# Kernel optimization log

Hardware: AMD Instinct MI355X
Metric: run time of the kernel (lower is better)

Reference implementation:

```python
import jax, jax.numpy as jnp
import numpy as np

NUM_HEADS = 16
HEAD_DIM = 64  # hidden_size 1024 / 16 heads


def setup_inputs() -> dict:
    key = jax.random.key(0)
    ks = jax.random.split(key, 4)
    B, S, H = 2, 2048, 1024
    scale = 0.02
    return {
        "hidden_states": jax.random.normal(ks[0], (B, S, H), jnp.float32),
        "attention_mask": jnp.zeros((B, 1, 1, S), jnp.float32),  # additive mask
        "Wq": jax.random.normal(ks[1], (H, H), jnp.float32) * scale,
        "bq": jnp.zeros((H,), jnp.float32),
        "Wk": jax.random.normal(ks[2], (H, H), jnp.float32) * scale,
        "bk": jnp.zeros((H,), jnp.float32),
        "Wv": jax.random.normal(ks[3], (H, H), jnp.float32) * scale,
        "bv": jnp.zeros((H,), jnp.float32),
    }


def _split_heads(x):
    B, S, H = x.shape
    return x.reshape(B, S, NUM_HEADS, HEAD_DIM).transpose(0, 2, 1, 3)  # [B,h,S,dh]


def reference(hidden_states, attention_mask, Wq, bq, Wk, bk, Wv, bv):
    q = _split_heads(hidden_states @ Wq + bq)
    k = _split_heads(hidden_states @ Wk + bk)
    v = _split_heads(hidden_states @ Wv + bv)
    # scaled dot-product scores [B,h,S,S]
    scores = jnp.einsum("bhqd,bhkd->bhqk", q, k) / np.sqrt(HEAD_DIM).astype(np.float32)
    scores = scores + attention_mask  # additive mask, broadcast [B,1,1,S]
    probs = jax.nn.softmax(scores, axis=-1)  # dropout prob = 0.0
    ctx = jnp.einsum("bhqk,bhkd->bhqd", probs, v)
    B, h, S, dh = ctx.shape
    return ctx.transpose(0, 2, 1, 3).reshape(B, S, h * dh)  # [B,S,hidden]
```

## Files before the change

### kernel.cpp

```cpp
#include <hip/hip_runtime.h>
#include <hip/hip_bf16.h>


typedef __bf16 bf16x8 __attribute__((ext_vector_type(8)));
typedef __bf16 bf16x4 __attribute__((ext_vector_type(4)));
typedef float f32x4 __attribute__((ext_vector_type(4)));
typedef float f32x16 __attribute__((ext_vector_type(16)));

static constexpr int H = 1024;
static constexpr int S = 2048;
static constexpr int NH = 16;
static constexpr int DH = 64;
static constexpr float L2E = 1.4426950408889634f;

#if __has_builtin(__builtin_amdgcn_exp2f)
#define EXP2F(x) __builtin_amdgcn_exp2f(x)
#else
#define EXP2F(x) __builtin_exp2f(x)
#endif

__device__ inline void gll16(const void* g, void* l) {
  __builtin_amdgcn_global_load_lds(
      (const __attribute__((address_space(1))) void*)g,
      (__attribute__((address_space(3))) void*)l, 16, 0, 0);
}

__global__ __launch_bounds__(256) void convert_kernel(
    const float* __restrict__ X, const float* __restrict__ W0,
    const float* __restrict__ W1, const float* __restrict__ W2,
    __bf16* __restrict__ Xb, __bf16* __restrict__ Wt) {
  __shared__ float T[64][65];
  const int bid = blockIdx.x, tid = threadIdx.x;
  if (bid < 2048) {
    size_t i = ((size_t)bid * 256 + tid) * 8;
    float4 f0 = *(const float4*)(X + i);
    float4 f1 = *(const float4*)(X + i + 4);
    bf16x8 o;
    o[0] = (__bf16)f0.x; o[1] = (__bf16)f0.y; o[2] = (__bf16)f0.z; o[3] = (__bf16)f0.w;
    o[4] = (__bf16)f1.x; o[5] = (__bf16)f1.y; o[6] = (__bf16)f1.z; o[7] = (__bf16)f1.w;
    *(bf16x8*)(Xb + i) = o;
    return;
  }
  const int wid = bid - 2048;
  const int z = wid >> 8, t = wid & 255;
  const int k0 = (t >> 4) * 64, n0 = (t & 15) * 64;
  const float* W = z == 0 ? W0 : (z == 1 ? W1 : W2);
  __bf16* Wo = Wt + (size_t)z * H * H;
#pragma unroll
  for (int it = 0; it < 4; ++it) {
    int r = it * 16 + (tid >> 4), c = (tid & 15) * 4;
    *(float4*)&T[r][c] = *(const float4*)&W[(size_t)(k0 + r) * H + n0 + c];
  }
  __syncthreads();
#pragma unroll
  for (int it = 0; it < 4; ++it) {
    int n = it * 16 + (tid >> 4), c0 = (tid & 15) * 4;
    bf16x4 o;
#pragma unroll
    for (int j = 0; j < 4; ++j) o[j] = (__bf16)T[c0 + j][n];
    *(bf16x4*)&Wo[(size_t)(n0 + n) * H + k0 + c0] = o;
  }
}

__global__ __launch_bounds__(256, 3) void qkv_gemm_kernel(
    const __bf16* __restrict__ Xb, const __bf16* __restrict__ Wt,
    const float* __restrict__ bq, const float* __restrict__ bk,
    const float* __restrict__ bv,
    __bf16* __restrict__ Qt, __bf16* __restrict__ K, __bf16* __restrict__ Vt)
{
  __shared__ __bf16 As[128 * 64];
  __shared__ __bf16 Bs[128 * 64];

  const int tid = threadIdx.x, lane = tid & 63, w = tid >> 6;
  const int quad = lane >> 4, l16 = lane & 15;
  const int wsel = blockIdx.x >> 3;
  const int n0 = (blockIdx.x & 7) * 128;
  const int m0 = blockIdx.y * 128;
  const int wr = w & 1, wc = w >> 1;

  const __bf16* Wsel = Wt + (size_t)wsel * H * H;
  const float* bias = wsel == 0 ? bq : (wsel == 1 ? bk : bv);

  const __bf16* aptr[4];
  const __bf16* bptr[4];
#pragma unroll
  for (int i = 0; i < 4; ++i) {
    int s = w * 256 + i * 64 + lane;
    int row = s >> 3, col = s & 7, sc = col ^ (row & 7);
    aptr[i] = Xb + (size_t)(m0 + row) * H + sc * 8;
    bptr[i] = Wsel + (size_t)(n0 + row) * H + sc * 8;
  }

  f32x4 acc[4][4] = {};

  for (int k0 = 0; k0 < H; k0 += 64) {
    __syncthreads();
#pragma unroll
    for (int i = 0; i < 4; ++i) {
      gll16(aptr[i] + k0, &As[(w * 256 + i * 64) * 8]);
      gll16(bptr[i] + k0, &Bs[(w * 256 + i * 64) * 8]);
    }
    __syncthreads();
#pragma unroll
    for (int kc = 0; kc < 2; ++kc) {
      bf16x8 af[4], bfr[4];
#pragma unroll
      for (int t = 0; t < 4; ++t) {
        int ra = wr * 64 + t * 16 + l16;
        af[t] = *(const bf16x8*)&As[ra * 64 + (((kc * 4 + quad) ^ (ra & 7)) * 8)];
        int rb = wc * 64 + t * 16 + l16;
        bfr[t] = *(const bf16x8*)&Bs[rb * 64 + (((kc * 4 + quad) ^ (rb & 7)) * 8)];
      }
#pragma unroll
      for (int t = 0; t < 4; ++t)
#pragma unroll
        for (int u = 0; u < 4; ++u)
          acc[t][u] = __builtin_amdgcn_mfma_f32_16x16x32_bf16(af[t], bfr[u], acc[t][u], 0, 0, 0);
    }
  }

  const float qscale = 0.125f * L2E;
#pragma unroll
  for (int u = 0; u < 4; ++u) {
    int n = n0 + wc * 64 + u * 16 + l16;
    int head = n >> 6, d = n & 63;
    float bias_v = bias[n];
#pragma unroll
    for (int t = 0; t < 4; ++t) {
      int srow = m0 + wr * 64 + t * 16 + quad * 4;
      int b = srow >> 11, si = srow & (S - 1);
      int bh = b * NH + head;
      if (wsel == 1) {
        __bf16* dst = K + ((size_t)bh * S + si) * DH + d;
#pragma unroll
        for (int r = 0; r < 4; ++r)
          dst[(size_t)r * DH] = (__bf16)(acc[t][u][r] + bias_v);
      } else {
        float scl = wsel == 0 ? qscale : 1.0f;
        __bf16* outp = wsel == 0 ? Qt : Vt;
        bf16x4 o;
#pragma unroll
        for (int r = 0; r < 4; ++r) o[r] = (__bf16)((acc[t][u][r] + bias_v) * scl);
        *(bf16x4*)&outp[((size_t)bh * DH + d) * S + si] = o;
      }
    }
  }
}

__global__ __launch_bounds__(256, 2) void attn_kernel(
    const __bf16* __restrict__ Qt, const __bf16* __restrict__ K,
    const __bf16* __restrict__ Vt, const float* __restrict__ mask,
    float* __restrict__ out)
{
  __shared__ __bf16 Ks[2][64 * 64];
  __shared__ __bf16 Vs[2][64 * 64];
  __shared__ float  Ms[S];
  __shared__ __bf16 Pb[4][32 * 64];

  const int tid = threadIdx.x, lane = tid & 63, w = tid >> 6;
  const int l31 = lane & 31, hi = lane >> 5;

  const int lin = blockIdx.y * 16 + blockIdx.x;
  const int v = (lin & 7) * 64 + (lin >> 3);
  const int bh = v >> 4, b = bh >> 4, h = bh & 15;
  const int q0 = (v & 15) * 128;

  const __bf16* Qb = Qt + (size_t)bh * DH * S;
  const __bf16* Kb = K + (size_t)bh * S * DH;
  const __bf16* Vb = Vt + (size_t)bh * DH * S;
  const float* mb = mask + (size_t)b * S;

  {
    int idx = tid * 8;
    float4 m0v = *(const float4*)&mb[idx];
    float4 m1v = *(const float4*)&mb[idx + 4];
    float4 s0v = {m0v.x * L2E, m0v.y * L2E, m0v.z * L2E, m0v.w * L2E};
    float4 s1v = {m1v.x * L2E, m1v.y * L2E, m1v.z * L2E, m1v.w * L2E};
    *(float4*)&Ms[idx] = s0v;
    *(float4*)&Ms[idx + 4] = s1v;
  }

  const int q = q0 + w * 32 + l31;
  bf16x8 qf[4];
#pragma unroll
  for (int kc = 0; kc < 4; ++kc)
#pragma unroll
    for (int j = 0; j < 8; ++j)
      qf[kc][j] = Qb[(size_t)(kc * 16 + hi * 8 + j) * S + q];

  const __bf16* kptr[2];
  const __bf16* vptr[2];
#pragma unroll
  for (int i = 0; i < 2; ++i) {
    int s = w * 128 + i * 64 + lane;
    int row = s >> 3, col = s & 7, sc = col ^ (row & 7);
    kptr[i] = Kb + (size_t)row * DH + sc * 8;
    vptr[i] = Vb + (size_t)row * S + sc * 8;
  }

#pragma unroll
  for (int i = 0; i < 2; ++i) {
    gll16(kptr[i], &Ks[0][(w * 128 + i * 64) * 8]);
    gll16(vptr[i], &Vs[0][(w * 128 + i * 64) * 8]);
  }

  f32x16 o0 = {}, o1 = {};
  float dl = 0.0f;
  int cur = 0;

  for (int kv0 = 0; kv0 < S; kv0 += 64) {
    __syncthreads();
    if (kv0 + 64 < S) {
      const int nxt = cur ^ 1;
#pragma unroll
      for (int i = 0; i < 2; ++i) {
        gll16(kptr[i] + (size_t)(kv0 + 64) * DH, &Ks[nxt][(w * 128 + i * 64) * 8]);
        gll16(vptr[i] + (kv0 + 64), &Vs[nxt][(w * 128 + i * 64) * 8]);
      }
    }

#pragma unroll
    for (int kvsub = 0; kvsub < 2; ++kvsub) {
      const int rk = kvsub * 32 + l31;
      f32x16 cc;
#pragma unroll
      for (int g = 0; g < 4; ++g) {
        float4 m4 = *(const float4*)&Ms[kv0 + kvsub * 32 + g * 8 + hi * 4];
        cc[4 * g + 0] = m4.x; cc[4 * g + 1] = m4.y;
        cc[4 * g + 2] = m4.z; cc[4 * g + 3] = m4.w;
      }
#pragma unroll
      for (int kc = 0; kc < 4; ++kc) {
        bf16x8 af = *(const bf16x8*)&Ks[cur][rk * 64 + (((kc * 2 + hi) ^ (l31 & 7)) * 8)];
        cc = __builtin_amdgcn_mfma_f32_32x32x16_bf16(af, qf[kc], cc, 0, 0, 0);
      }
#pragma unroll
      for (int g = 0; g < 4; ++g) {
        bf16x4 pk;
#pragma unroll
        for (int r = 0; r < 4; ++r) {
          float p = EXP2F(cc[4 * g + r]);
          pk[r] = (__bf16)p;
          dl += (float)pk[r];
        }
        int ccn = kvsub * 4 + g;
        *(bf16x4*)&Pb[w][l31 * 64 + ((ccn ^ (l31 & 7)) * 8) + hi * 4] = pk;
      }
    }

    bf16x8 pf[4];
#pragma unroll
    for (int pc = 0; pc < 4; ++pc)
      pf[pc] = *(const bf16x8*)&Pb[w][l31 * 64 + (((pc * 2 + hi) ^ (l31 & 7)) * 8)];
#pragma unroll
    for (int pc = 0; pc < 4; ++pc) {
      bf16x8 vf0 = *(const bf16x8*)&Vs[cur][l31 * 64 + (((pc * 2 + hi) ^ (l31 & 7)) * 8)];
      o0 = __builtin_amdgcn_mfma_f32_32x32x16_bf16(vf0, pf[pc], o0, 0, 0, 0);
      bf16x8 vf1 = *(const bf16x8*)&Vs[cur][(32 + l31) * 64 + (((pc * 2 + hi) ^ (l31 & 7)) * 8)];
      o1 = __builtin_amdgcn_mfma_f32_32x32x16_bf16(vf1, pf[pc], o1, 0, 0, 0);
    }
    cur ^= 1;
  }

  float lsum = dl + __shfl_xor(dl, 32);
  float invl = 1.0f / lsum;

#pragma unroll
  for (int g = 0; g < 4; ++g) {
    int d0 = g * 8 + hi * 4;
    float4 s0 = {o0[4 * g + 0] * invl, o0[4 * g + 1] * invl,
                 o0[4 * g + 2] * invl, o0[4 * g + 3] * invl};
    *(float4*)&out[((size_t)b * S + q) * H + h * DH + d0] = s0;
    float4 s1 = {o1[4 * g + 0] * invl, o1[4 * g + 1] * invl,
                 o1[4 * g + 2] * invl, o1[4 * g + 3] * invl};
    *(float4*)&out[((size_t)b * S + q) * H + h * DH + 32 + d0] = s1;
  }
}

extern "C" void kernel_launch(void* const* d_in, const int* in_sizes, int n_in,
                              void* d_out, int out_size, void* d_ws, size_t ws_size,
                              hipStream_t stream) {
  const float* X    = (const float*)d_in[0];
  const float* mask = (const float*)d_in[1];
  const float* Wq   = (const float*)d_in[2];
  const float* bq   = (const float*)d_in[3];
  const float* Wk   = (const float*)d_in[4];
  const float* bk   = (const float*)d_in[5];
  const float* Wv   = (const float*)d_in[6];
  const float* bv   = (const float*)d_in[7];
  float* out = (float*)d_out;

  const size_t per = (size_t)2 * NH * S * DH;
  __bf16* Qws  = (__bf16*)d_ws;
  __bf16* Kws  = Qws + per;
  __bf16* Vtws = Kws + per;

  __bf16* Xb = (__bf16*)d_out;
  __bf16* Wt = Xb + per;

  convert_kernel<<<2816, 256, 0, stream>>>(X, Wq, Wk, Wv, Xb, Wt);
  qkv_gemm_kernel<<<dim3(24, 32), 256, 0, stream>>>(Xb, Wt, bq, bk, bv,
                                                    Qws, Kws, Vtws);
  attn_kernel<<<dim3(16, 32), 256, 0, stream>>>(Qws, Kws, Vtws, mask, out);
}
```

Measured before the change: 173.8 us.

## Split KV range across two wave groups and pass P through registers via permlane swap

The attention block grows to 512 threads. Two groups of four waves each process half of the KV sequence and their partial outputs and row sums are merged through LDS at the end. The P matrix is no longer staged through LDS; it is packed into bf16 pairs and rearranged across lanes with v_permlane32_swap so it can feed the PV MFMA directly. s_setprio hints are added around the MFMA sections. The aim is more waves in flight per query tile and less LDS traffic, at the cost of an extra reduction step, more LDS per block, and tighter register limits from launch_bounds(512,4).

```diff
diff --git a/kernel.cpp b/kernel.cpp
--- a/kernel.cpp
+++ b/kernel.cpp
@@ -6,6 +6,7 @@
 typedef __bf16 bf16x4 __attribute__((ext_vector_type(4)));
 typedef float f32x4 __attribute__((ext_vector_type(4)));
 typedef float f32x16 __attribute__((ext_vector_type(16)));
+typedef int i32x4 __attribute__((ext_vector_type(4)));
 
 static constexpr int H = 1024;
 static constexpr int S = 2048;
@@ -23,6 +24,16 @@
   __builtin_amdgcn_global_load_lds(
       (const __attribute__((address_space(1))) void*)g,
       (__attribute__((address_space(3))) void*)l, 16, 0, 0);
+}
+
+__device__ inline int pack2bf(float lo, float hi) {
+  unsigned short a = __builtin_bit_cast(unsigned short, (__bf16)lo);
+  unsigned short b = __builtin_bit_cast(unsigned short, (__bf16)hi);
+  return (int)(((unsigned)b << 16) | (unsigned)a);
+}
+
+__device__ inline void plswap(int& a, int& b) {
+  asm volatile("v_permlane32_swap_b32 %0, %1" : "+v"(a), "+v"(b));
 }
 
 __global__ __launch_bounds__(256) void convert_kernel(
@@ -147,18 +158,18 @@
   }
 }
 
-__global__ __launch_bounds__(256, 2) void attn_kernel(
+__global__ __launch_bounds__(512, 4) void attn_kernel(
     const __bf16* __restrict__ Qt, const __bf16* __restrict__ K,
     const __bf16* __restrict__ Vt, const float* __restrict__ mask,
     float* __restrict__ out)
 {
-  __shared__ __bf16 Ks[2][64 * 64];
-  __shared__ __bf16 Vs[2][64 * 64];
+  __shared__ __bf16 Ks[2][2][64 * 64];
+  __shared__ __bf16 Vs[2][2][64 * 64];
   __shared__ float  Ms[S];
-  __shared__ __bf16 Pb[4][32 * 64];
 
   const int tid = threadIdx.x, lane = tid & 63, w = tid >> 6;
   const int l31 = lane & 31, hi = lane >> 5;
+  const int wl = w & 3, wh = w >> 2;
 
   const int lin = blockIdx.y * 16 + blockIdx.x;
   const int v = (lin & 7) * 64 + (lin >> 3);
@@ -171,16 +182,13 @@
   const float* mb = mask + (size_t)b * S;
 
   {
-    int idx = tid * 8;
-    float4 m0v = *(const float4*)&mb[idx];
-    float4 m1v = *(const float4*)&mb[idx + 4];
-    float4 s0v = {m0v.x * L2E, m0v.y * L2E, m0v.z * L2E, m0v.w * L2E};
-    float4 s1v = {m1v.x * L2E, m1v.y * L2E, m1v.z * L2E, m1v.w * L2E};
-    *(float4*)&Ms[idx] = s0v;
-    *(float4*)&Ms[idx + 4] = s1v;
-  }
-
-  const int q = q0 + w * 32 + l31;
+    int idx = tid * 4;
+    float4 mv = *(const float4*)&mb[idx];
+    float4 sv = {mv.x * L2E, mv.y * L2E, mv.z * L2E, mv.w * L2E};
+    *(float4*)&Ms[idx] = sv;
+  }
+
+  const int q = q0 + wl * 32 + l31;
   bf16x8 qf[4];
 #pragma unroll
   for (int kc = 0; kc < 4; ++kc)
@@ -188,36 +196,40 @@
     for (int j = 0; j < 8; ++j)
       qf[kc][j] = Qb[(size_t)(kc * 16 + hi * 8 + j) * S + q];
 
+  const int kvbase = wh * 1024;
   const __bf16* kptr[2];
   const __bf16* vptr[2];
 #pragma unroll
   for (int i = 0; i < 2; ++i) {
-    int s = w * 128 + i * 64 + lane;
+    int s = wl * 128 + i * 64 + lane;
     int row = s >> 3, col = s & 7, sc = col ^ (row & 7);
-    kptr[i] = Kb + (size_t)row * DH + sc * 8;
-    vptr[i] = Vb + (size_t)row * S + sc * 8;
+    kptr[i] = Kb + (size_t)(kvbase + row) * DH + sc * 8;
+    vptr[i] = Vb + (size_t)row * S + kvbase + sc * 8;
   }
 
 #pragma unroll
   for (int i = 0; i < 2; ++i) {
-    gll16(kptr[i], &Ks[0][(w * 128 + i * 64) * 8]);
-    gll16(vptr[i], &Vs[0][(w * 128 + i * 64) * 8]);
+    gll16(kptr[i], &Ks[wh][0][(wl * 128 + i * 64 + lane) * 8]);
+    gll16(vptr[i], &Vs[wh][0][(wl * 128 + i * 64 + lane) * 8]);
   }
 
   f32x16 o0 = {}, o1 = {};
   float dl = 0.0f;
   int cur = 0;
 
-  for (int kv0 = 0; kv0 < S; kv0 += 64) {
+  for (int st = 0; st < 16; ++st) {
     __syncthreads();
-    if (kv0 + 64 < S) {
+    if (st + 1 < 16) {
       const int nxt = cur ^ 1;
 #pragma unroll
       for (int i = 0; i < 2; ++i) {
-        gll16(kptr[i] + (size_t)(kv0 + 64) * DH, &Ks[nxt][(w * 128 + i * 64) * 8]);
-        gll16(vptr[i] + (kv0 + 64), &Vs[nxt][(w * 128 + i * 64) * 8]);
-      }
-    }
+        gll16(kptr[i] + (size_t)(st + 1) * 64 * DH, &Ks[wh][nxt][(wl * 128 + i * 64 + lane) * 8]);
+        gll16(vptr[i] + (st + 1) * 64, &Vs[wh][nxt][(wl * 128 + i * 64 + lane) * 8]);
+      }
+    }
+    const __bf16* Kc = &Ks[wh][cur][0];
+    const __bf16* Vc = &Vs[wh][cur][0];
+    const int kvabs = kvbase + st * 64;
 
 #pragma unroll
     for (int kvsub = 0; kvsub < 2; ++kvsub) {
@@ -225,55 +237,82 @@
       f32x16 cc;
 #pragma unroll
       for (int g = 0; g < 4; ++g) {
-        float4 m4 = *(const float4*)&Ms[kv0 + kvsub * 32 + g * 8 + hi * 4];
+        float4 m4 = *(const float4*)&Ms[kvabs + kvsub * 32 + g * 8 + hi * 4];
         cc[4 * g + 0] = m4.x; cc[4 * g + 1] = m4.y;
         cc[4 * g + 2] = m4.z; cc[4 * g + 3] = m4.w;
       }
+      __builtin_amdgcn_s_setprio(1);
 #pragma unroll
       for (int kc = 0; kc < 4; ++kc) {
-        bf16x8 af = *(const bf16x8*)&Ks[cur][rk * 64 + (((kc * 2 + hi) ^ (l31 & 7)) * 8)];
+        bf16x8 af = *(const bf16x8*)&Kc[rk * 64 + (((kc * 2 + hi) ^ (l31 & 7)) * 8)];
         cc = __builtin_amdgcn_mfma_f32_32x32x16_bf16(af, qf[kc], cc, 0, 0, 0);
       }
-#pragma unroll
-      for (int g = 0; g < 4; ++g) {
-        bf16x4 pk;
-#pragma unroll
-        for (int r = 0; r < 4; ++r) {
-          float p = EXP2F(cc[4 * g + r]);
-          pk[r] = (__bf16)p;
-          dl += (float)pk[r];
-        }
-        int ccn = kvsub * 4 + g;
-        *(bf16x4*)&Pb[w][l31 * 64 + ((ccn ^ (l31 & 7)) * 8) + hi * 4] = pk;
-      }
-    }
-
-    bf16x8 pf[4];
-#pragma unroll
-    for (int pc = 0; pc < 4; ++pc)
-      pf[pc] = *(const bf16x8*)&Pb[w][l31 * 64 + (((pc * 2 + hi) ^ (l31 & 7)) * 8)];
-#pragma unroll
-    for (int pc = 0; pc < 4; ++pc) {
-      bf16x8 vf0 = *(const bf16x8*)&Vs[cur][l31 * 64 + (((pc * 2 + hi) ^ (l31 & 7)) * 8)];
-      o0 = __builtin_amdgcn_mfma_f32_32x32x16_bf16(vf0, pf[pc], o0, 0, 0, 0);
-      bf16x8 vf1 = *(const bf16x8*)&Vs[cur][(32 + l31) * 64 + (((pc * 2 + hi) ^ (l31 & 7)) * 8)];
-      o1 = __builtin_amdgcn_mfma_f32_32x32x16_bf16(vf1, pf[pc], o1, 0, 0, 0);
+      __builtin_amdgcn_s_setprio(0);
+
+      float p[16];
+#pragma unroll
+      for (int r = 0; r < 16; ++r) { p[r] = EXP2F(cc[r]); dl += p[r]; }
+      int a0 = pack2bf(p[0],  p[1]),  b0 = pack2bf(p[2],  p[3]);
+      int a1 = pack2bf(p[4],  p[5]),  b1 = pack2bf(p[6],  p[7]);
+      int a2 = pack2bf(p[8],  p[9]),  b2 = pack2bf(p[10], p[11]);
+      int a3 = pack2bf(p[12], p[13]), b3 = pack2bf(p[14], p[15]);
+      plswap(a0, a1); plswap(b0, b1);
+      plswap(a2, a3); plswap(b2, b3);
+      i32x4 pi0 = {a0, b0, a1, b1};
+      i32x4 pi1 = {a2, b2, a3, b3};
+      bf16x8 pf0 = __builtin_bit_cast(bf16x8, pi0);
+      bf16x8 pf1 = __builtin_bit_cast(bf16x8, pi1);
+
+      __builtin_amdgcn_s_setprio(1);
+#pragma unroll
+      for (int pp = 0; pp < 2; ++pp) {
+        const int pc = kvsub * 2 + pp;
+        const bf16x8 pf = pp ? pf1 : pf0;
+        bf16x8 vf0 = *(const bf16x8*)&Vc[l31 * 64 + (((pc * 2 + hi) ^ (l31 & 7)) * 8)];
+        o0 = __builtin_amdgcn_mfma_f32_32x32x16_bf16(vf0, pf, o0, 0, 0, 0);
+        bf16x8 vf1 = *(const bf16x8*)&Vc[(32 + l31) * 64 + (((pc * 2 + hi) ^ (l31 & 7)) * 8)];
+        o1 = __builtin_amdgcn_mfma_f32_32x32x16_bf16(vf1, pf, o1, 0, 0, 0);
+      }
+      __builtin_amdgcn_s_setprio(0);
     }
     cur ^= 1;
   }
 
   float lsum = dl + __shfl_xor(dl, 32);
-  float invl = 1.0f / lsum;
-
-#pragma unroll
-  for (int g = 0; g < 4; ++g) {
-    int d0 = g * 8 + hi * 4;
-    float4 s0 = {o0[4 * g + 0] * invl, o0[4 * g + 1] * invl,
-                 o0[4 * g + 2] * invl, o0[4 * g + 3] * invl};
-    *(float4*)&out[((size_t)b * S + q) * H + h * DH + d0] = s0;
-    float4 s1 = {o1[4 * g + 0] * invl, o1[4 * g + 1] * invl,
-                 o1[4 * g + 2] * invl, o1[4 * g + 3] * invl};
-    *(float4*)&out[((size_t)b * S + q) * H + h * DH + 32 + d0] = s1;
+
+  __syncthreads();
+  float* Os = (float*)&Ks[0][0][0];
+  float* Ls = (float*)&Vs[0][0][0];
+  if (wh == 1) {
+#pragma unroll
+    for (int g = 0; g < 4; ++g) {
+      int s0 = (2 * g + hi) ^ (l31 & 7);
+      float4 t0 = {o0[4 * g + 0], o0[4 * g + 1], o0[4 * g + 2], o0[4 * g + 3]};
+      *(float4*)&Os[(wl * 32 + l31) * 64 + s0 * 4] = t0;
+      int s1 = (8 + 2 * g + hi) ^ (l31 & 7);
+      float4 t1 = {o1[4 * g + 0], o1[4 * g + 1], o1[4 * g + 2], o1[4 * g + 3]};
+      *(float4*)&Os[(wl * 32 + l31) * 64 + s1 * 4] = t1;
+    }
+    if (hi == 0) Ls[wl * 32 + l31] = lsum;
+  }
+  __syncthreads();
+  if (wh == 0) {
+    float ltot = lsum + Ls[wl * 32 + l31];
+    float invl = 1.0f / ltot;
+#pragma unroll
+    for (int g = 0; g < 4; ++g) {
+      int d0 = g * 8 + hi * 4;
+      int s0 = (2 * g + hi) ^ (l31 & 7);
+      float4 u0 = *(const float4*)&Os[(wl * 32 + l31) * 64 + s0 * 4];
+      float4 r0 = {(o0[4 * g + 0] + u0.x) * invl, (o0[4 * g + 1] + u0.y) * invl,
+                   (o0[4 * g + 2] + u0.z) * invl, (o0[4 * g + 3] + u0.w) * invl};
+      *(float4*)&out[((size_t)b * S + q) * H + h * DH + d0] = r0;
+      int s1 = (8 + 2 * g + hi) ^ (l31 & 7);
+      float4 u1 = *(const float4*)&Os[(wl * 32 + l31) * 64 + s1 * 4];
+      float4 r1 = {(o1[4 * g + 0] + u1.x) * invl, (o1[4 * g + 1] + u1.y) * invl,
+                   (o1[4 * g + 2] + u1.z) * invl, (o1[4 * g + 3] + u1.w) * invl};
+      *(float4*)&out[((size_t)b * S + q) * H + h * DH + 32 + d0] = r1;
+    }
   }
 }
 
@@ -301,5 +340,5 @@
   convert_kernel<<<2816, 256, 0, stream>>>(X, Wq, Wk, Wv, Xb, Wt);
   qkv_gemm_kernel<<<dim3(24, 32), 256, 0, stream>>>(Xb, Wt, bq, bk, bv,
                                                     Qws, Kws, Vtws);
-  attn_kernel<<<dim3(16, 32), 256, 0, stream>>>(Qws, Kws, Vtws, mask, out);
-}
+  attn_kernel<<<dim3(16, 32), 512, 0, stream>>>(Qws, Kws, Vtws, mask, out);
+}
```

Result: faster. 170.1 us (-2.1%).
